# Optimization experiments

Measured on AMD Instinct MI355X. Metric: run time of the kernel, lower is better.

Reference implementation:

```python
import jax, jax.numpy as jnp
import numpy as np

EPS = 1e-5
CONV_THRESHOLD = 0.0


def setup_inputs() -> dict:
    key = jax.random.key(0)
    ks = jax.random.split(key, 16)
    B, F = 65536, 256
    H1, H2 = 1024, 512
    d_in = F + 1  # raw features + 1 scalar conv feature
    inp = {
        "x": jax.random.normal(ks[0], (B, F), dtype=jnp.float32),
        # layer 1: Linear(d_in, H1) + BatchNorm1d(H1)
        "W1": jax.random.normal(ks[1], (d_in, H1), dtype=jnp.float32) * (1.0 / np.sqrt(d_in)),
        "b1": jax.random.normal(ks[2], (H1,), dtype=jnp.float32) * 0.01,
        "g1": jnp.ones((H1,), jnp.float32) + 0.1 * jax.random.normal(ks[3], (H1,), dtype=jnp.float32),
        "be1": jax.random.normal(ks[4], (H1,), dtype=jnp.float32) * 0.01,
        "m1": jax.random.normal(ks[5], (H1,), dtype=jnp.float32) * 0.1,
        "v1": jax.random.uniform(ks[6], (H1,), dtype=jnp.float32, minval=0.5, maxval=1.5),
        # layer 2: Linear(H1, H2) + BatchNorm1d(H2)
        "W2": jax.random.normal(ks[7], (H1, H2), dtype=jnp.float32) * (1.0 / np.sqrt(H1)),
        "b2": jax.random.normal(ks[8], (H2,), dtype=jnp.float32) * 0.01,
        "g2": jnp.ones((H2,), jnp.float32) + 0.1 * jax.random.normal(ks[9], (H2,), dtype=jnp.float32),
        "be2": jax.random.normal(ks[10], (H2,), dtype=jnp.float32) * 0.01,
        "m2": jax.random.normal(ks[11], (H2,), dtype=jnp.float32) * 0.1,
        "v2": jax.random.uniform(ks[12], (H2,), dtype=jnp.float32, minval=0.5, maxval=1.5),
        # output head: Linear(H2, 1)
        "W3": jax.random.normal(ks[13], (H2, 1), dtype=jnp.float32) * (1.0 / np.sqrt(H2)),
        "b3": jax.random.normal(ks[14], (1,), dtype=jnp.float32) * 0.01,
    }
    return inp


def _bn(h, g, be, m, v):
    # eval-mode BatchNorm1d with running statistics
    return g * (h - m) * jax.lax.rsqrt(v + EPS) + be


def reference(x, W1, b1, g1, be1, m1, v1, W2, b2, g2, be2, m2, v2, W3, b3):
    # Batched replacement of the per-sample numpy threshold conv:
    # the Conv filter reduces the whole sample patch with a mean and thresholds it,
    # producing one binary scalar feature per sample.  [B, 1]
    conv_feat = jnp.where(jnp.mean(x, axis=1, keepdims=True) > CONV_THRESHOLD, 1.0, 0.0).astype(x.dtype)
    h = jnp.concatenate([x, conv_feat], axis=1)  # [B, F+1]
    h = jax.nn.relu(_bn(h @ W1 + b1, g1, be1, m1, v1))  # [B, H1]
    h = jax.nn.relu(_bn(h @ W2 + b2, g2, be2, m2, v2))  # [B, H2]
    return jax.nn.sigmoid(h @ W3 + b3)  # [B, 1]
```

## Files before the change

### kernel.cpp

```cpp
#include <hip/hip_runtime.h>
#include <hip/hip_bf16.h>
#include <cstdint>
#include <cstddef>

typedef __bf16 bf16_t;
typedef bf16_t bf16x8 __attribute__((ext_vector_type(8)));
typedef float f32x4 __attribute__((ext_vector_type(4)));

#define BN_EPS 1e-5f

__device__ __forceinline__ void async_load16(const bf16_t* g, bf16_t* lds) {
  __builtin_amdgcn_global_load_lds(
      (__attribute__((address_space(1))) uint32_t*)(g),
      (__attribute__((address_space(3))) uint32_t*)(lds),
      16, 0, 0);
}

__global__ void prep_weights_kernel(const float* __restrict__ W1, const float* __restrict__ W2,
                                    const float* b1, const float* g1, const float* be1,
                                    const float* m1, const float* v1,
                                    const float* b2, const float* g2, const float* be2,
                                    const float* m2, const float* v2,
                                    bf16_t* __restrict__ W1T, bf16_t* __restrict__ W2T,
                                    float* s1, float* t1, float* s2, float* t2,
                                    float* w1last) {
  const int b = blockIdx.x;
  if (b < 192) {
    const float* src;
    bf16_t* dst;
    int R, C, bx, by;
    if (b < 64) { src = W1; dst = W1T; R = 256; C = 1024; bx = b & 15; by = b >> 4; }
    else        { src = W2; dst = W2T; R = 1024; C = 512; bx = (b - 64) & 7; by = (b - 64) >> 3; }
    __shared__ bf16_t tile[64][66];
    const int r0 = by * 64, c0 = bx * 64;
    const int tc = threadIdx.x & 63;
    const int tr4 = threadIdx.x >> 6;
#pragma unroll
    for (int i = 0; i < 16; ++i) {
      int r = i * 4 + tr4;
      tile[r][tc] = (bf16_t)src[(size_t)(r0 + r) * C + c0 + tc];
    }
    __syncthreads();
#pragma unroll
    for (int i = 0; i < 16; ++i) {
      int rr = i * 4 + tr4;
      dst[(size_t)(c0 + rr) * R + r0 + tc] = tile[tc][rr];
    }
  } else {
    for (int i = threadIdx.x; i < 1024; i += 256) {
      float s = g1[i] * rsqrtf(v1[i] + BN_EPS);
      s1[i] = s;
      t1[i] = be1[i] - m1[i] * s + b1[i] * s;
      w1last[i] = W1[256 * 1024 + i];
      if (i < 512) {
        float s2v = g2[i] * rsqrtf(v2[i] + BN_EPS);
        s2[i] = s2v;
        t2[i] = be2[i] - m2[i] * s2v + b2[i] * s2v;
      }
    }
  }
}

__global__ __launch_bounds__(1024, 4) void fused_mlp(
    const float* __restrict__ x,
    const bf16_t* __restrict__ W1T, const bf16_t* __restrict__ W2T,
    const float* __restrict__ s1, const float* __restrict__ t1,
    const float* __restrict__ w1last,
    const float* __restrict__ s2, const float* __restrict__ t2,
    const float* __restrict__ W3, const float* __restrict__ b3,
    float* __restrict__ out) {
  __shared__ __align__(16) unsigned char smem[131072];
  const int tid = threadIdx.x;
  const int lane = tid & 63;
  const int w = tid >> 6;
  const int l15 = lane & 15;
  const int quad = lane >> 4;
  const int mTile = blockIdx.x * 64;

  bf16_t* As = (bf16_t*)smem;
  bf16_t* h1c = (bf16_t*)(smem + 32768);
  float* convs = (float*)(smem + 32768);
  bf16_t* B1s = (bf16_t*)(smem + 65536);
  float* outW = (float*)(smem + 65536);

  {
    const int rsub = lane >> 5;
    const int cc = lane & 31;
#pragma unroll
    for (int i = 0; i < 2; ++i) {
      int row = w * 4 + i * 2 + rsub;
      const float* gx = x + (size_t)(mTile + row) * 256 + cc * 8;
      const float4 a = *(const float4*)gx;
      const float4 bq = *(const float4*)(gx + 4);
      float s = a.x + a.y + a.z + a.w + bq.x + bq.y + bq.z + bq.w;
      bf16x8 v = {(bf16_t)a.x, (bf16_t)a.y, (bf16_t)a.z, (bf16_t)a.w,
                  (bf16_t)bq.x, (bf16_t)bq.y, (bf16_t)bq.z, (bf16_t)bq.w};
      *(bf16x8*)(As + row * 256 + (cc ^ (row & 7)) * 8) = v;
#pragma unroll
      for (int m = 1; m <= 16; m <<= 1) s += __shfl_xor(s, m);
      if (cc == 0) convs[row] = (s > 0.0f) ? 1.0f : 0.0f;
    }
  }
  __syncthreads();

  unsigned cmask = 0;
#pragma unroll
  for (int ti = 0; ti < 4; ++ti)
#pragma unroll
    for (int r = 0; r < 4; ++r)
      if (convs[ti * 16 + quad * 4 + r] > 0.5f) cmask |= (1u << (ti * 4 + r));

  bf16_t* B1w = B1s + w * 2048;
  const int srow = lane >> 2;
  const int schunk = (lane & 3) ^ ((lane >> 3) & 3);
  const int rchunk = quad ^ ((l15 >> 1) & 3);

  f32x4 acc2[4][2];
#pragma unroll
  for (int i = 0; i < 4; ++i)
#pragma unroll
    for (int j = 0; j < 2; ++j) {
      f32x4 z = {0.f, 0.f, 0.f, 0.f};
      acc2[i][j] = z;
    }

  for (int c = 0; c < 4; ++c) {
    const int colbase = c * 256 + w * 16;
    f32x4 acc1[4];
#pragma unroll
    for (int i = 0; i < 4; ++i) {
      f32x4 z = {0.f, 0.f, 0.f, 0.f};
      acc1[i] = z;
    }

    const bf16_t* gB1 = W1T + (size_t)(colbase + srow) * 256 + schunk * 8;

#pragma unroll
    for (int p = 0; p < 4; ++p)
      async_load16(gB1 + p * 32, B1w + p * 512 + lane * 8);

#pragma unroll
    for (int ks = 0; ks < 8; ++ks) {
      if (ks < 5)      asm volatile("s_waitcnt vmcnt(3)" ::: "memory");
      else if (ks == 5) asm volatile("s_waitcnt vmcnt(2)" ::: "memory");
      else if (ks == 6) asm volatile("s_waitcnt vmcnt(1)" ::: "memory");
      else              asm volatile("s_waitcnt vmcnt(0)" ::: "memory");
      __builtin_amdgcn_sched_barrier(0);

      bf16x8 bfr = *(const bf16x8*)(B1w + (ks & 3) * 512 + l15 * 32 + rchunk * 8);
      bf16x8 af[4];
#pragma unroll
      for (int ti = 0; ti < 4; ++ti)
        af[ti] = *(const bf16x8*)(As + (ti * 16 + l15) * 256 +
                                  ((ks * 4 + quad) ^ (l15 & 7)) * 8);

      asm volatile("s_waitcnt lgkmcnt(0)" ::: "memory");
      __builtin_amdgcn_sched_barrier(0);
      if (ks < 4)
        async_load16(gB1 + (ks + 4) * 32, B1w + (ks & 3) * 512 + lane * 8);

      __builtin_amdgcn_s_setprio(1);
#pragma unroll
      for (int ti = 0; ti < 4; ++ti)
        acc1[ti] = __builtin_amdgcn_mfma_f32_16x16x32_bf16(af[ti], bfr, acc1[ti], 0, 0, 0);
      __builtin_amdgcn_s_setprio(0);
    }

    __syncthreads();

    {
      const int ccol = colbase + l15;
      const float sc1 = s1[ccol];
      const float tc1 = t1[ccol];
      const float wl1 = w1last[ccol];
      const int colc = w * 16 + l15;
#pragma unroll
      for (int ti = 0; ti < 4; ++ti)
#pragma unroll
        for (int r = 0; r < 4; ++r) {
          const int rowl = ti * 16 + quad * 4 + r;
          const float cfv = ((cmask >> (ti * 4 + r)) & 1u) ? 1.0f : 0.0f;
          float z = acc1[ti][r] + cfv * wl1;
          z = fmaxf(z * sc1 + tc1, 0.f);
          const int c8 = (colc >> 3) ^ (rowl & 7);
          h1c[rowl * 256 + c8 * 8 + (l15 & 7)] = (bf16_t)z;
        }
    }
    __syncthreads();

#pragma unroll
    for (int s = 0; s < 8; ++s) {
      bf16x8 bfr2[2];
#pragma unroll
      for (int tj = 0; tj < 2; ++tj)
        bfr2[tj] = *(const bf16x8*)(W2T + (size_t)(w * 32 + tj * 16 + l15) * 1024 +
                                    c * 256 + s * 32 + quad * 8);
#pragma unroll
      for (int ti = 0; ti < 4; ++ti) {
        bf16x8 af2 = *(const bf16x8*)(h1c + (ti * 16 + l15) * 256 +
                                      ((s * 4 + quad) ^ (l15 & 7)) * 8);
        __builtin_amdgcn_s_setprio(1);
        acc2[ti][0] = __builtin_amdgcn_mfma_f32_16x16x32_bf16(af2, bfr2[0], acc2[ti][0], 0, 0, 0);
        acc2[ti][1] = __builtin_amdgcn_mfma_f32_16x16x32_bf16(af2, bfr2[1], acc2[ti][1], 0, 0, 0);
        __builtin_amdgcn_s_setprio(0);
      }
    }
  }

  float sc[2], tcs[2], w3c[2];
#pragma unroll
  for (int tj = 0; tj < 2; ++tj) {
    int ccol = w * 32 + tj * 16 + l15;
    sc[tj] = s2[ccol];
    tcs[tj] = t2[ccol];
    w3c[tj] = W3[ccol];
  }
#pragma unroll
  for (int ti = 0; ti < 4; ++ti)
#pragma unroll
    for (int r = 0; r < 4; ++r) {
      float pv = 0.f;
#pragma unroll
      for (int tj = 0; tj < 2; ++tj) {
        float z = fmaxf(acc2[ti][tj][r] * sc[tj] + tcs[tj], 0.f);
        pv += z * w3c[tj];
      }
#pragma unroll
      for (int m = 1; m <= 8; m <<= 1) pv += __shfl_xor(pv, m);
      if (l15 == 0)
        outW[w * 64 + ti * 16 + quad * 4 + r] = pv;
    }
  __syncthreads();
  if (tid < 64) {
    float z = b3[0];
#pragma unroll
    for (int k = 0; k < 16; ++k) z += outW[k * 64 + tid];
    out[mTile + tid] = 1.0f / (1.0f + expf(-z));
  }
}

extern "C" void kernel_launch(void* const* d_in, const int* in_sizes, int n_in,
                              void* d_out, int out_size, void* d_ws, size_t ws_size,
                              hipStream_t stream) {
  const float* x = (const float*)d_in[0];
  const float* W1 = (const float*)d_in[1];
  const float* b1 = (const float*)d_in[2];
  const float* g1 = (const float*)d_in[3];
  const float* be1 = (const float*)d_in[4];
  const float* m1 = (const float*)d_in[5];
  const float* v1 = (const float*)d_in[6];
  const float* W2 = (const float*)d_in[7];
  const float* b2 = (const float*)d_in[8];
  const float* g2 = (const float*)d_in[9];
  const float* be2 = (const float*)d_in[10];
  const float* m2 = (const float*)d_in[11];
  const float* v2 = (const float*)d_in[12];
  const float* W3 = (const float*)d_in[13];
  const float* b3 = (const float*)d_in[14];
  float* out = (float*)d_out;

  char* p = (char*)d_ws;
  bf16_t* h1 = (bf16_t*)p;       p += (size_t)65536 * 1024 * 2;
  float* partials = (float*)p;   p += (size_t)4 * 65536 * 4;
  bf16_t* W1T = (bf16_t*)p;      p += (size_t)1024 * 256 * 2;
  bf16_t* W2T = (bf16_t*)p;      p += (size_t)512 * 1024 * 2;
  float* w1last = (float*)p;     p += 1024 * 4;
  float* s1 = (float*)p;         p += 1024 * 4;
  float* t1 = (float*)p;         p += 1024 * 4;
  float* s2 = (float*)p;         p += 512 * 4;
  float* t2 = (float*)p;         p += 512 * 4;
  (void)h1;
  (void)partials;

  prep_weights_kernel<<<193, 256, 0, stream>>>(W1, W2, b1, g1, be1, m1, v1,
                                               b2, g2, be2, m2, v2,
                                               W1T, W2T, s1, t1, s2, t2, w1last);

  fused_mlp<<<1024, 1024, 0, stream>>>(x, W1T, W2T, s1, t1, w1last,
                                       s2, t2, W3, b3, out);
}
```

Measured before the change: 300.4 us.

## Switch fused MLP to 32x32x16 MFMA with 512-column h1 chunks

```diff
diff --git a/kernel.cpp b/kernel.cpp
--- a/kernel.cpp
+++ b/kernel.cpp
@@ -5,7 +5,7 @@
 
 typedef __bf16 bf16_t;
 typedef bf16_t bf16x8 __attribute__((ext_vector_type(8)));
-typedef float f32x4 __attribute__((ext_vector_type(4)));
+typedef float f32x16 __attribute__((ext_vector_type(16)));
 
 #define BN_EPS 1e-5f
 
@@ -73,15 +73,15 @@
   const int tid = threadIdx.x;
   const int lane = tid & 63;
   const int w = tid >> 6;
-  const int l15 = lane & 15;
-  const int quad = lane >> 4;
+  const int l31 = lane & 31;
+  const int half = lane >> 5;
   const int mTile = blockIdx.x * 64;
 
   bf16_t* As = (bf16_t*)smem;
   bf16_t* h1c = (bf16_t*)(smem + 32768);
   float* convs = (float*)(smem + 32768);
-  bf16_t* B1s = (bf16_t*)(smem + 65536);
-  float* outW = (float*)(smem + 65536);
+  bf16_t* B1s = (bf16_t*)(smem + 98304);
+  float* outW = (float*)(smem + 98304);
 
   {
     const int rsub = lane >> 5;
@@ -105,131 +105,111 @@
 
   unsigned cmask = 0;
 #pragma unroll
-  for (int ti = 0; ti < 4; ++ti)
-#pragma unroll
-    for (int r = 0; r < 4; ++r)
-      if (convs[ti * 16 + quad * 4 + r] > 0.5f) cmask |= (1u << (ti * 4 + r));
-
-  bf16_t* B1w = B1s + w * 2048;
-  const int srow = lane >> 2;
-  const int schunk = (lane & 3) ^ ((lane >> 3) & 3);
-  const int rchunk = quad ^ ((l15 >> 1) & 3);
-
-  f32x4 acc2[4][2];
-#pragma unroll
-  for (int i = 0; i < 4; ++i)
-#pragma unroll
-    for (int j = 0; j < 2; ++j) {
-      f32x4 z = {0.f, 0.f, 0.f, 0.f};
-      acc2[i][j] = z;
-    }
-
-  for (int c = 0; c < 4; ++c) {
-    const int colbase = c * 256 + w * 16;
-    f32x4 acc1[4];
-#pragma unroll
-    for (int i = 0; i < 4; ++i) {
-      f32x4 z = {0.f, 0.f, 0.f, 0.f};
-      acc1[i] = z;
-    }
-
-    const bf16_t* gB1 = W1T + (size_t)(colbase + srow) * 256 + schunk * 8;
-
-#pragma unroll
-    for (int p = 0; p < 4; ++p)
-      async_load16(gB1 + p * 32, B1w + p * 512 + lane * 8);
-
-#pragma unroll
-    for (int ks = 0; ks < 8; ++ks) {
-      if (ks < 5)      asm volatile("s_waitcnt vmcnt(3)" ::: "memory");
-      else if (ks == 5) asm volatile("s_waitcnt vmcnt(2)" ::: "memory");
-      else if (ks == 6) asm volatile("s_waitcnt vmcnt(1)" ::: "memory");
-      else              asm volatile("s_waitcnt vmcnt(0)" ::: "memory");
+  for (int t = 0; t < 2; ++t)
+#pragma unroll
+    for (int q = 0; q < 4; ++q)
+#pragma unroll
+      for (int m = 0; m < 4; ++m)
+        if (convs[t * 32 + q * 8 + m + 4 * half] > 0.5f)
+          cmask |= 1u << (t * 16 + q * 4 + m);
+
+  bf16_t* B1w = B1s + w * 1024;
+  const int brd = (l31 * 2 + half) * 8;
+
+  f32x16 acc2[2];
+#pragma unroll
+  for (int t = 0; t < 2; ++t)
+#pragma unroll
+    for (int i = 0; i < 16; ++i) acc2[t][i] = 0.f;
+
+  for (int c = 0; c < 2; ++c) {
+    const int colbase = c * 512 + w * 32;
+    f32x16 acc1[2];
+#pragma unroll
+    for (int t = 0; t < 2; ++t)
+#pragma unroll
+      for (int i = 0; i < 16; ++i) acc1[t][i] = 0.f;
+
+    const bf16_t* gB1 = W1T + (size_t)(colbase + (lane >> 1)) * 256 + (lane & 1) * 8;
+
+    async_load16(gB1, B1w + lane * 8);
+    async_load16(gB1 + 16, B1w + 512 + lane * 8);
+
+#pragma unroll
+    for (int ks = 0; ks < 16; ++ks) {
+      if (ks < 15) asm volatile("s_waitcnt vmcnt(1)" ::: "memory");
+      else         asm volatile("s_waitcnt vmcnt(0)" ::: "memory");
       __builtin_amdgcn_sched_barrier(0);
 
-      bf16x8 bfr = *(const bf16x8*)(B1w + (ks & 3) * 512 + l15 * 32 + rchunk * 8);
-      bf16x8 af[4];
-#pragma unroll
-      for (int ti = 0; ti < 4; ++ti)
-        af[ti] = *(const bf16x8*)(As + (ti * 16 + l15) * 256 +
-                                  ((ks * 4 + quad) ^ (l15 & 7)) * 8);
+      bf16x8 bfr = *(const bf16x8*)(B1w + (ks & 1) * 512 + brd);
+      bf16x8 af0 = *(const bf16x8*)(As + l31 * 256 + ((ks * 2 + half) ^ (l31 & 7)) * 8);
+      bf16x8 af1 = *(const bf16x8*)(As + (l31 + 32) * 256 + ((ks * 2 + half) ^ (l31 & 7)) * 8);
 
       asm volatile("s_waitcnt lgkmcnt(0)" ::: "memory");
       __builtin_amdgcn_sched_barrier(0);
-      if (ks < 4)
-        async_load16(gB1 + (ks + 4) * 32, B1w + (ks & 3) * 512 + lane * 8);
+      if (ks < 14)
+        async_load16(gB1 + (ks + 2) * 16, B1w + (ks & 1) * 512 + lane * 8);
 
       __builtin_amdgcn_s_setprio(1);
-#pragma unroll
-      for (int ti = 0; ti < 4; ++ti)
-        acc1[ti] = __builtin_amdgcn_mfma_f32_16x16x32_bf16(af[ti], bfr, acc1[ti], 0, 0, 0);
+      acc1[0] = __builtin_amdgcn_mfma_f32_32x32x16_bf16(af0, bfr, acc1[0], 0, 0, 0);
+      acc1[1] = __builtin_amdgcn_mfma_f32_32x32x16_bf16(af1, bfr, acc1[1], 0, 0, 0);
       __builtin_amdgcn_s_setprio(0);
     }
 
     __syncthreads();
 
     {
-      const int ccol = colbase + l15;
+      const int ccol = colbase + l31;
       const float sc1 = s1[ccol];
       const float tc1 = t1[ccol];
       const float wl1 = w1last[ccol];
-      const int colc = w * 16 + l15;
-#pragma unroll
-      for (int ti = 0; ti < 4; ++ti)
-#pragma unroll
-        for (int r = 0; r < 4; ++r) {
-          const int rowl = ti * 16 + quad * 4 + r;
-          const float cfv = ((cmask >> (ti * 4 + r)) & 1u) ? 1.0f : 0.0f;
-          float z = acc1[ti][r] + cfv * wl1;
+      const int cc2 = w * 4 + (l31 >> 3);
+      const int j = lane & 7;
+#pragma unroll
+      for (int t = 0; t < 2; ++t)
+#pragma unroll
+        for (int r = 0; r < 16; ++r) {
+          const int row = (r & 3) + 8 * (r >> 2) + 4 * half + t * 32;
+          const float cfv = ((cmask >> (t * 16 + (r >> 2) * 4 + (r & 3))) & 1u) ? 1.0f : 0.0f;
+          float z = acc1[t][r] + cfv * wl1;
           z = fmaxf(z * sc1 + tc1, 0.f);
-          const int c8 = (colc >> 3) ^ (rowl & 7);
-          h1c[rowl * 256 + c8 * 8 + (l15 & 7)] = (bf16_t)z;
+          h1c[row * 512 + (cc2 ^ (row & 7)) * 8 + j] = (bf16_t)z;
         }
     }
     __syncthreads();
 
-#pragma unroll
-    for (int s = 0; s < 8; ++s) {
-      bf16x8 bfr2[2];
-#pragma unroll
-      for (int tj = 0; tj < 2; ++tj)
-        bfr2[tj] = *(const bf16x8*)(W2T + (size_t)(w * 32 + tj * 16 + l15) * 1024 +
-                                    c * 256 + s * 32 + quad * 8);
-#pragma unroll
-      for (int ti = 0; ti < 4; ++ti) {
-        bf16x8 af2 = *(const bf16x8*)(h1c + (ti * 16 + l15) * 256 +
-                                      ((s * 4 + quad) ^ (l15 & 7)) * 8);
-        __builtin_amdgcn_s_setprio(1);
-        acc2[ti][0] = __builtin_amdgcn_mfma_f32_16x16x32_bf16(af2, bfr2[0], acc2[ti][0], 0, 0, 0);
-        acc2[ti][1] = __builtin_amdgcn_mfma_f32_16x16x32_bf16(af2, bfr2[1], acc2[ti][1], 0, 0, 0);
-        __builtin_amdgcn_s_setprio(0);
+    const bf16_t* gB2 = W2T + (size_t)(w * 32 + l31) * 1024 + c * 512 + half * 8;
+    bf16x8 bcur = *(const bf16x8*)(gB2);
+#pragma unroll
+    for (int s = 0; s < 32; ++s) {
+      bf16x8 bnxt;
+      if (s < 31) bnxt = *(const bf16x8*)(gB2 + (s + 1) * 16);
+      bf16x8 a0 = *(const bf16x8*)(h1c + l31 * 512 + ((s * 2 + half) ^ (l31 & 7)) * 8);
+      bf16x8 a1 = *(const bf16x8*)(h1c + (l31 + 32) * 512 + ((s * 2 + half) ^ (l31 & 7)) * 8);
+      __builtin_amdgcn_s_setprio(1);
+      acc2[0] = __builtin_amdgcn_mfma_f32_32x32x16_bf16(a0, bcur, acc2[0], 0, 0, 0);
+      acc2[1] = __builtin_amdgcn_mfma_f32_32x32x16_bf16(a1, bcur, acc2[1], 0, 0, 0);
+      __builtin_amdgcn_s_setprio(0);
+      if (s < 31) bcur = bnxt;
+    }
+  }
+
+  {
+    const int ncol = w * 32 + l31;
+    const float sc = s2[ncol];
+    const float tcs = t2[ncol];
+    const float w3c = W3[ncol];
+#pragma unroll
+    for (int t = 0; t < 2; ++t)
+#pragma unroll
+      for (int r = 0; r < 16; ++r) {
+        float z = fmaxf(acc2[t][r] * sc + tcs, 0.f) * w3c;
+#pragma unroll
+        for (int m = 1; m <= 16; m <<= 1) z += __shfl_xor(z, m);
+        if (l31 == 0)
+          outW[w * 64 + t * 32 + (r & 3) + 8 * (r >> 2) + 4 * half] = z;
       }
-    }
-  }
-
-  float sc[2], tcs[2], w3c[2];
-#pragma unroll
-  for (int tj = 0; tj < 2; ++tj) {
-    int ccol = w * 32 + tj * 16 + l15;
-    sc[tj] = s2[ccol];
-    tcs[tj] = t2[ccol];
-    w3c[tj] = W3[ccol];
-  }
-#pragma unroll
-  for (int ti = 0; ti < 4; ++ti)
-#pragma unroll
-    for (int r = 0; r < 4; ++r) {
-      float pv = 0.f;
-#pragma unroll
-      for (int tj = 0; tj < 2; ++tj) {
-        float z = fmaxf(acc2[ti][tj][r] * sc[tj] + tcs[tj], 0.f);
-        pv += z * w3c[tj];
-      }
-#pragma unroll
-      for (int m = 1; m <= 8; m <<= 1) pv += __shfl_xor(pv, m);
-      if (l15 == 0)
-        outW[w * 64 + ti * 16 + quad * 4 + r] = pv;
-    }
+  }
   __syncthreads();
   if (tid < 64) {
     float z = b3[0];
```

After: 476.1 us. +58.5%, slower.
